# Performance work log

Hardware: AMD Instinct MI355X
Metric: run time of the kernel (lower is better)

The kernel has to match this reference:

```python
import jax, jax.numpy as jnp
import numpy as np

N, E = 50000, 400000          # nodes, edges
T, R = 4, 8                   # node types, relations (edge types)
H, DK = 8, 32                 # heads, head dim
DIN = DOUT = 256              # in/out feature dim (DOUT = H*DK)
SQRT_DK = float(np.sqrt(DK))


def setup_inputs() -> dict:
    key = jax.random.key(0)
    ks = jax.random.split(key, 12)
    f32 = jnp.float32
    return {
        "x": jax.random.normal(ks[0], (N, DIN), f32),
        "node_type": jax.random.randint(ks[1], (N,), 0, T, jnp.int32),
        "src": jax.random.randint(ks[2], (E,), 0, N, jnp.int32),
        "dst": jax.random.randint(ks[3], (E,), 0, N, jnp.int32),
        "etype": jax.random.randint(ks[4], (E,), 0, R, jnp.int32),
        "Wk": jax.random.normal(ks[5], (T, DOUT, DIN), f32) / np.sqrt(DIN).astype(np.float32),
        "bk": jnp.zeros((T, DOUT), f32),
        "Wq": jax.random.normal(ks[6], (T, DOUT, DIN), f32) / np.sqrt(DIN).astype(np.float32),
        "bq": jnp.zeros((T, DOUT), f32),
        "Wv": jax.random.normal(ks[7], (T, DOUT, DIN), f32) / np.sqrt(DIN).astype(np.float32),
        "bv": jnp.zeros((T, DOUT), f32),
        "Wa": jax.random.normal(ks[8], (T, DOUT, DOUT), f32) / np.sqrt(DOUT).astype(np.float32),
        "ba": jnp.zeros((T, DOUT), f32),
        "rel_pri": jnp.ones((R, H), f32),
        "rel_att": jax.random.normal(ks[9], (R, H, DK, DK), f32) / np.sqrt(DK).astype(np.float32),  # ~xavier
        "rel_msg": jax.random.normal(ks[10], (R, H, DK, DK), f32) / np.sqrt(DK).astype(np.float32),
        "skip": jnp.ones((T,), f32),
    }


def _typed_linear(h, W, b, ntype):
    # per-node-type linear: y_n = W[type_n] @ h_n + b[type_n]
    y = jnp.einsum('ni,tdi->ntd', h, W)                      # [N,T,D] (T is small)
    y = jnp.take_along_axis(y, ntype[:, None, None], axis=1)[:, 0]
    return y + b[ntype]


def _hgt_forward(x, node_type, src, dst, etype,
                 Wk, bk, Wq, bq, Wv, bv, Wa, ba,
                 rel_pri, rel_att, rel_msg, skip):
    # typed k/q/v projections -> [N,H,DK]
    K = _typed_linear(x, Wk, bk, node_type).reshape(N, H, DK)
    Q = _typed_linear(x, Wq, bq, node_type).reshape(N, H, DK)
    V = _typed_linear(x, Wv, bv, node_type).reshape(N, H, DK)

    k_e, q_e, v_e = K[src], Q[dst], V[src]                   # [E,H,DK] gathers

    # per-relation head transforms (loop over small fixed R, masked accumulate)
    key_e = jnp.zeros_like(k_e)
    msg_e = jnp.zeros_like(v_e)
    for r in range(R):
        m = (etype == r)[:, None, None].astype(x.dtype)
        key_e = key_e + m * jnp.einsum('ehd,hdf->ehf', k_e, rel_att[r])
        msg_e = msg_e + m * jnp.einsum('ehd,hdf->ehf', v_e, rel_msg[r])

    att = (q_e * key_e).sum(-1) * rel_pri[etype] / SQRT_DK   # [E,H]

    # softmax per (dst node, edge type) segment, then mean across edge types
    seg = dst * R + etype                                    # [E]
    S = N * R
    amax = jax.ops.segment_max(att, seg, num_segments=S)     # [S,H]
    ex = jnp.exp(att - amax[seg])
    denom = jax.ops.segment_sum(ex, seg, num_segments=S)
    w = ex / denom[seg]                                      # normalized attention [E,H]
    h_seg = jax.ops.segment_sum(w[:, :, None] * msg_e, seg, num_segments=S)  # [S,H,DK]
    cnt = jax.ops.segment_sum(jnp.ones((E,), x.dtype), seg, num_segments=S)  # [S]

    h_nr = h_seg.reshape(N, R, DOUT)
    present = (cnt.reshape(N, R) > 0).astype(x.dtype)        # which etypes hit each node
    t = h_nr.sum(1) / jnp.maximum(present.sum(1), 1.0)[:, None]  # cross_reducer='mean'

    trans = _typed_linear(t, Wa, ba, node_type)              # per-type output linear
    alpha = jax.nn.sigmoid(skip)[node_type][:, None]
    return trans * alpha + x * (1.0 - alpha)


def reference(x, node_type, src, dst, etype,
              Wk, bk, Wq, bq, Wv, bv, Wa, ba,
              rel_pri, rel_att, rel_msg, skip):
    return _hgt_forward(x, node_type, src, dst, etype,
                        Wk, bk, Wq, bq, Wv, bv, Wa, ba,
                        rel_pri, rel_att, rel_msg, skip)
```

## Files before the change

### kernel.cpp

```cpp
#include <hip/hip_runtime.h>
#include <math.h>
#include <stdint.h>

#define N_NODES 50000
#define N_EDGES 400000
#define N_T 4
#define N_R 8
#define N_H 8
#define DKD 32
#define D 256
#define TM 64
#define N_SEG (N_NODES * N_R)
#define EMASK 0xFFFFF
#define PROJ_BLOCKS ((N_NODES + TM - 1) / TM + N_T)

typedef _Float16 h2 __attribute__((ext_vector_type(2)));
typedef _Float16 v8h __attribute__((ext_vector_type(8)));
typedef float v4f __attribute__((ext_vector_type(4)));
typedef unsigned short u16;

__device__ __forceinline__ u16 h2u(_Float16 h) { return __builtin_bit_cast(u16, h); }
__device__ __forceinline__ h2 u2h2(unsigned int u) { return __builtin_bit_cast(h2, u); }

#if __has_builtin(__builtin_amdgcn_fdot2)
__device__ __forceinline__ float fdot2f(h2 a, h2 b, float c) {
    return __builtin_amdgcn_fdot2(a, b, c, false);
}
#else
__device__ __forceinline__ float fdot2f(h2 a, h2 b, float c) {
    return c + (float)a[0] * (float)b[0] + (float)a[1] * (float)b[1];
}
#endif

__device__ __forceinline__ float dot32h(const uint4* __restrict__ a,
                                        const uint4* __restrict__ q) {
    float s = 0.f;
    #pragma unroll
    for (int j = 0; j < 4; j++) {
        uint4 av = a[j], qv = q[j];
        s = fdot2f(u2h2(av.x), u2h2(qv.x), s);
        s = fdot2f(u2h2(av.y), u2h2(qv.y), s);
        s = fdot2f(u2h2(av.z), u2h2(qv.z), s);
        s = fdot2f(u2h2(av.w), u2h2(qv.w), s);
    }
    return s;
}

__global__ __launch_bounds__(256) void k_cvtW(
    const float4* __restrict__ w0, const float4* __restrict__ w1,
    const float4* __restrict__ w2, const float4* __restrict__ w3,
    ushort4* __restrict__ d, int n4each) {
    int i = blockIdx.x * 256 + threadIdx.x;
    if (i >= 4 * n4each) return;
    int sel = i / n4each, j = i - sel * n4each;
    const float4* s = (sel == 0) ? w0 : (sel == 1) ? w1 : (sel == 2) ? w2 : w3;
    float4 v = s[j];
    ushort4 o;
    o.x = h2u((_Float16)v.x); o.y = h2u((_Float16)v.y);
    o.z = h2u((_Float16)v.z); o.w = h2u((_Float16)v.w);
    d[i] = o;
}

__global__ __launch_bounds__(256) void k_cvt_att(const float4* __restrict__ s,
                                                 const float* __restrict__ pri,
                                                 ushort4* __restrict__ d, int n4) {
    int i = blockIdx.x * 256 + threadIdx.x;
    if (i >= n4) return;
    int mat = i >> 8;
    float sc = pri[mat] * 0.17677669529663687f;
    float4 v = s[i];
    ushort4 o;
    o.x = h2u((_Float16)(v.x * sc)); o.y = h2u((_Float16)(v.y * sc));
    o.z = h2u((_Float16)(v.z * sc)); o.w = h2u((_Float16)(v.w * sc));
    d[i] = o;
}

__global__ __launch_bounds__(256) void k_cvt_t(const float* __restrict__ s,
                                               u16* __restrict__ d) {
    int i = blockIdx.x * 256 + threadIdx.x;
    if (i >= N_R * N_H * DKD * DKD) return;
    int mat = i >> 10, w = i & 1023;
    int d0 = w >> 5, f = w & 31;
    d[(mat << 10) + f * DKD + d0] = h2u((_Float16)s[i]);
}

__global__ void k_hist(const int* __restrict__ nt, int* __restrict__ cnt) {
    int n = blockIdx.x * blockDim.x + threadIdx.x;
    if (n < N_NODES) atomicAdd(&cnt[nt[n]], 1);
}

__global__ void k_scan(const int* __restrict__ cnt, int* __restrict__ off,
                       int* __restrict__ toff) {
    int o = 0, to = 0;
    for (int t = 0; t < N_T; t++) {
        off[t] = o; toff[t] = to;
        o += cnt[t]; to += (cnt[t] + TM - 1) / TM;
    }
    off[N_T] = o; toff[N_T] = to;
}

__global__ void k_scatter(const int* __restrict__ nt, const int* __restrict__ off,
                          int* __restrict__ cur, int* __restrict__ order) {
    int n = blockIdx.x * blockDim.x + threadIdx.x;
    if (n >= N_NODES) return;
    int t = nt[n];
    int pos = off[t] + atomicAdd(&cur[t], 1);
    order[pos] = n;
}

__global__ void k_hist_seg(const int* __restrict__ dst, const int* __restrict__ et,
                           int* __restrict__ cnt) {
    int e = blockIdx.x * blockDim.x + threadIdx.x;
    if (e < N_EDGES) atomicAdd(&cnt[dst[e] * N_R + et[e]], 1);
}

__global__ __launch_bounds__(1024) void k_scan_l1(const int* __restrict__ cnt,
                                                  int* __restrict__ excl,
                                                  int* __restrict__ bsum) {
    __shared__ int sh[1024];
    int tid = threadIdx.x, i = blockIdx.x * 1024 + tid;
    int v = (i < N_SEG) ? cnt[i] : 0;
    sh[tid] = v;
    __syncthreads();
    #pragma unroll
    for (int ofs = 1; ofs < 1024; ofs <<= 1) {
        int t = (tid >= ofs) ? sh[tid - ofs] : 0;
        __syncthreads();
        sh[tid] += t;
        __syncthreads();
    }
    if (i < N_SEG) excl[i] = sh[tid] - v;
    if (tid == 1023) bsum[blockIdx.x] = sh[1023];
}

__global__ __launch_bounds__(512) void k_scan_l2(int* __restrict__ bsum, int NB) {
    __shared__ int sh[512];
    int tid = threadIdx.x;
    int v = (tid < NB) ? bsum[tid] : 0;
    sh[tid] = v;
    __syncthreads();
    #pragma unroll
    for (int ofs = 1; ofs < 512; ofs <<= 1) {
        int t = (tid >= ofs) ? sh[tid - ofs] : 0;
        __syncthreads();
        sh[tid] += t;
        __syncthreads();
    }
    if (tid < NB) bsum[tid] = sh[tid] - v;
}

__global__ void k_scan_l3(int* __restrict__ excl, const int* __restrict__ bsum) {
    int i = blockIdx.x * blockDim.x + threadIdx.x;
    if (i < N_SEG) excl[i] += bsum[i >> 10];
    else if (i == N_SEG) excl[N_SEG] = N_EDGES;
}

__global__ void k_scatter_seg(const int* __restrict__ src, const int* __restrict__ dst,
                              const int* __restrict__ et, const int* __restrict__ rp,
                              int* __restrict__ cur, int* __restrict__ esrc) {
    int e = blockIdx.x * blockDim.x + threadIdx.x;
    if (e >= N_EDGES) return;
    int r = et[e];
    int sg = dst[e] * N_R + r;
    int pos = rp[sg] + atomicAdd(&cur[sg], 1);
    esrc[pos] = src[e] | (r << 20);
}

__global__ __launch_bounds__(256) void k_proj(
    const float* __restrict__ x, const int* __restrict__ order,
    const int* __restrict__ off, const int* __restrict__ toff,
    const u16* __restrict__ Wkb, const float* __restrict__ bk,
    const u16* __restrict__ Wqb, const float* __restrict__ bq,
    const u16* __restrict__ Wvb, const float* __restrict__ bv,
    u16* __restrict__ Kb, u16* __restrict__ Qb, u16* __restrict__ Vb) {
    __shared__ __align__(16) u16 xs[TM][D + 8];
    int b = blockIdx.x;
    int t = -1;
    #pragma unroll
    for (int i = 0; i < N_T; i++)
        if (b >= toff[i] && b < toff[i + 1]) t = i;
    if (t < 0) return;
    int nodeBase = off[t] + (b - toff[t]) * TM;
    int count = min(TM, off[t + 1] - nodeBase);
    int tid = threadIdx.x;

    for (int j = tid; j < TM * (D / 4); j += 256) {
        int row = j >> 6, ch = j & 63;
        float4 v = {0.f, 0.f, 0.f, 0.f};
        if (row < count) {
            int g = order[nodeBase + row];
            v = *(const float4*)(x + (size_t)g * D + ch * 4);
        }
        ushort4 o;
        o.x = h2u((_Float16)v.x); o.y = h2u((_Float16)v.y);
        o.z = h2u((_Float16)v.z); o.w = h2u((_Float16)v.w);
        *(ushort4*)&xs[row][ch * 4] = o;
    }
    __syncthreads();

    int lane = tid & 63, wave = tid >> 6;
    int m = lane & 15, quad = lane >> 4;
    v8h a[8];
    #pragma unroll
    for (int ks = 0; ks < 8; ks++)
        a[ks] = *(const v8h*)&xs[wave * 16 + m][ks * 32 + quad * 8];

    int grow[4]; bool vrow[4];
    #pragma unroll
    for (int r = 0; r < 4; r++) {
        int rowi = wave * 16 + quad * 4 + r;
        vrow[r] = (rowi < count);
        grow[r] = vrow[r] ? order[nodeBase + rowi] : 0;
    }

    const u16* Ws[3] = {Wkb + (size_t)t * D * D, Wqb + (size_t)t * D * D, Wvb + (size_t)t * D * D};
    const float* Bs[3] = {bk + t * D, bq + t * D, bv + t * D};
    u16* Os[3] = {Kb, Qb, Vb};

    for (int p = 0; p < 3; p++) {
        const u16* W = Ws[p];
        for (int dt = 0; dt < 16; dt++) {
            int dcol = dt * 16 + m;
            v4f acc = {0.f, 0.f, 0.f, 0.f};
            #pragma unroll
            for (int ks = 0; ks < 8; ks++) {
                v8h bf = *(const v8h*)(W + (size_t)dcol * D + ks * 32 + quad * 8);
                acc = __builtin_amdgcn_mfma_f32_16x16x32_f16(a[ks], bf, acc, 0, 0, 0);
            }
            float bias = Bs[p][dcol];
            #pragma unroll
            for (int r = 0; r < 4; r++) {
                if (vrow[r])
                    Os[p][(size_t)grow[r] * D + dcol] = h2u((_Float16)(acc[r] + bias));
            }
        }
    }
}

__global__ __launch_bounds__(256, 4) void k_fused(
    const u16* __restrict__ Kb, u16* QTb, const u16* __restrict__ Vb,
    const int* __restrict__ rowptr, const int* __restrict__ esrc,
    const u16* __restrict__ Ab, const u16* __restrict__ Mtb) {
    __shared__ __align__(16) unsigned int Uldu[4][N_H][20];
    int wave = threadIdx.x >> 6, lane = threadIdx.x & 63;
    int n = blockIdx.x * 4 + wave;
    if (n >= N_NODES) return;
    int h = lane >> 3, fl = lane & 7, fo = fl * 4;
    int base = n * N_R;

    int bnd[N_R + 1];
    #pragma unroll
    for (int i = 0; i <= N_R; i++) bnd[i] = rowptr[base + i];

    uint4 qv4[4];
    {
        const uint4* qp = (const uint4*)(QTb + (size_t)n * D + h * DKD);
        #pragma unroll
        for (int j = 0; j < 4; j++) qv4[j] = qp[j];
    }

    h2 qt2[N_R][2];
    int np = 0;
    #pragma unroll
    for (int r = 0; r < N_R; r++) {
        if (bnd[r] >= bnd[r + 1]) continue;
        np++;
        const u16* Ar = Ab + ((size_t)(r * N_H + h) * DKD + fo) * DKD;
        float q0 = dot32h((const uint4*)(Ar), qv4);
        float q1 = dot32h((const uint4*)(Ar + DKD), qv4);
        float q2 = dot32h((const uint4*)(Ar + 2 * DKD), qv4);
        float q3 = dot32h((const uint4*)(Ar + 3 * DKD), qv4);
        qt2[r][0] = h2{(_Float16)q0, (_Float16)q1};
        qt2[r][1] = h2{(_Float16)q2, (_Float16)q3};
    }

    float den[N_R] = {0.f, 0.f, 0.f, 0.f, 0.f, 0.f, 0.f, 0.f};
    float ua[N_R][4] = {};

#define DOTQ(P, RS, KU) { \
    h2 _ka = u2h2((KU).x), _kb = u2h2((KU).y); \
    switch (RS) { \
    case 0: P = fdot2f(_kb, qt2[0][1], fdot2f(_ka, qt2[0][0], 0.f)); break; \
    case 1: P = fdot2f(_kb, qt2[1][1], fdot2f(_ka, qt2[1][0], 0.f)); break; \
    case 2: P = fdot2f(_kb, qt2[2][1], fdot2f(_ka, qt2[2][0], 0.f)); break; \
    case 3: P = fdot2f(_kb, qt2[3][1], fdot2f(_ka, qt2[3][0], 0.f)); break; \
    case 4: P = fdot2f(_kb, qt2[4][1], fdot2f(_ka, qt2[4][0], 0.f)); break; \
    case 5: P = fdot2f(_kb, qt2[5][1], fdot2f(_ka, qt2[5][0], 0.f)); break; \
    case 6: P = fdot2f(_kb, qt2[6][1], fdot2f(_ka, qt2[6][0], 0.f)); break; \
    default: P = fdot2f(_kb, qt2[7][1], fdot2f(_ka, qt2[7][0], 0.f)); break; } }

#define ACCR(R, EX, V0, V1, V2, V3) \
    den[R] += EX; ua[R][0] += EX*V0; ua[R][1] += EX*V1; ua[R][2] += EX*V2; ua[R][3] += EX*V3;

#define ACCE(RS, EX, VU) { \
    h2 _va = u2h2((VU).x), _vb = u2h2((VU).y); \
    float _v0 = (float)_va[0], _v1 = (float)_va[1]; \
    float _v2 = (float)_vb[0], _v3 = (float)_vb[1]; \
    switch (RS) { \
    case 0: ACCR(0, EX, _v0, _v1, _v2, _v3) break; \
    case 1: ACCR(1, EX, _v0, _v1, _v2, _v3) break; \
    case 2: ACCR(2, EX, _v0, _v1, _v2, _v3) break; \
    case 3: ACCR(3, EX, _v0, _v1, _v2, _v3) break; \
    case 4: ACCR(4, EX, _v0, _v1, _v2, _v3) break; \
    case 5: ACCR(5, EX, _v0, _v1, _v2, _v3) break; \
    case 6: ACCR(6, EX, _v0, _v1, _v2, _v3) break; \
    default: ACCR(7, EX, _v0, _v1, _v2, _v3) break; } }

    int eb = bnd[0], ee = bnd[N_R];
    size_t hoff = (size_t)(h * DKD + fo);
    for (int w0 = eb; w0 < ee; w0 += 64) {
        int wcnt = min(64, ee - w0);
        int myek = (lane < wcnt) ? esrc[w0 + lane] : 0;
        for (int i0 = 0; i0 < wcnt; i0 += 4) {
            int mc = wcnt - i0;
            int pk0 = __shfl(myek, i0);
            int pk1 = __shfl(myek, i0 + (mc > 1 ? 1 : 0));
            int pk2 = __shfl(myek, i0 + (mc > 2 ? 2 : 0));
            int pk3 = __shfl(myek, i0 + (mc > 3 ? 3 : 0));
            int s0 = pk0 & EMASK, s1 = pk1 & EMASK, s2 = pk2 & EMASK, s3 = pk3 & EMASK;
            int r0 = __builtin_amdgcn_readfirstlane(pk0) >> 20;
            int r1 = __builtin_amdgcn_readfirstlane(pk1) >> 20;
            int r2 = __builtin_amdgcn_readfirstlane(pk2) >> 20;
            int r3 = __builtin_amdgcn_readfirstlane(pk3) >> 20;
            uint2 ku0 = *(const uint2*)(Kb + (size_t)s0 * D + hoff);
            uint2 ku1 = *(const uint2*)(Kb + (size_t)s1 * D + hoff);
            uint2 ku2 = *(const uint2*)(Kb + (size_t)s2 * D + hoff);
            uint2 ku3 = *(const uint2*)(Kb + (size_t)s3 * D + hoff);
            uint2 vu0 = *(const uint2*)(Vb + (size_t)s0 * D + hoff);
            uint2 vu1 = *(const uint2*)(Vb + (size_t)s1 * D + hoff);
            uint2 vu2 = *(const uint2*)(Vb + (size_t)s2 * D + hoff);
            uint2 vu3 = *(const uint2*)(Vb + (size_t)s3 * D + hoff);
            float p0, p1, p2, p3;
            DOTQ(p0, r0, ku0);
            DOTQ(p1, r1, ku1);
            DOTQ(p2, r2, ku2);
            DOTQ(p3, r3, ku3);
            p0 += __shfl_xor(p0, 1); p1 += __shfl_xor(p1, 1);
            p2 += __shfl_xor(p2, 1); p3 += __shfl_xor(p3, 1);
            p0 += __shfl_xor(p0, 2); p1 += __shfl_xor(p1, 2);
            p2 += __shfl_xor(p2, 2); p3 += __shfl_xor(p3, 2);
            p0 += __shfl_xor(p0, 4); p1 += __shfl_xor(p1, 4);
            p2 += __shfl_xor(p2, 4); p3 += __shfl_xor(p3, 4);
            float ex0 = __expf(p0), ex1 = __expf(p1);
            float ex2 = __expf(p2), ex3 = __expf(p3);
            ACCE(r0, ex0, vu0);
            if (mc > 1) { ACCE(r1, ex1, vu1); }
            if (mc > 2) { ACCE(r2, ex2, vu2); }
            if (mc > 3) { ACCE(r3, ex3, vu3); }
        }
    }

    float macc[4] = {0.f, 0.f, 0.f, 0.f};
    #pragma unroll
    for (int r = 0; r < N_R; r++) {
        if (bnd[r] >= bnd[r + 1]) continue;
        float invd = 1.f / den[r];
        unsigned int pw0 = __builtin_bit_cast(unsigned int,
            h2{(_Float16)(ua[r][0] * invd), (_Float16)(ua[r][1] * invd)});
        unsigned int pw1 = __builtin_bit_cast(unsigned int,
            h2{(_Float16)(ua[r][2] * invd), (_Float16)(ua[r][3] * invd)});
        __builtin_amdgcn_wave_barrier();
        *(uint2*)&Uldu[wave][h][fl * 2] = uint2{pw0, pw1};
        __builtin_amdgcn_wave_barrier();
        uint4 Um[4];
        #pragma unroll
        for (int j = 0; j < 4; j++)
            Um[j] = *(const uint4*)&Uldu[wave][h][4 * j];
        const u16* mp = Mtb + ((size_t)(r * N_H + h) * DKD + fo) * DKD;
        #pragma unroll
        for (int j = 0; j < 4; j++)
            macc[j] += dot32h((const uint4*)(mp + j * DKD), Um);
        __builtin_amdgcn_wave_barrier();
    }

    float invp = (np > 0) ? 1.f / (float)np : 1.f;
    ushort4 o;
    o.x = h2u((_Float16)(macc[0] * invp)); o.y = h2u((_Float16)(macc[1] * invp));
    o.z = h2u((_Float16)(macc[2] * invp)); o.w = h2u((_Float16)(macc[3] * invp));
    *(ushort4*)(QTb + (size_t)n * D + hoff) = o;
}

__global__ __launch_bounds__(256) void k_out(
    const u16* __restrict__ TBF, const float* __restrict__ x,
    const int* __restrict__ order, const int* __restrict__ off, const int* __restrict__ toff,
    const u16* __restrict__ Wab, const float* __restrict__ ba,
    const float* __restrict__ skip, float* __restrict__ out) {
    __shared__ __align__(16) u16 xs[TM][D + 8];
    int b = blockIdx.x;
    int t = -1;
    #pragma unroll
    for (int i = 0; i < N_T; i++)
        if (b >= toff[i] && b < toff[i + 1]) t = i;
    if (t < 0) return;
    int nodeBase = off[t] + (b - toff[t]) * TM;
    int count = min(TM, off[t + 1] - nodeBase);
    int tid = threadIdx.x;

    for (int j = tid; j < TM * 32; j += 256) {
        int row = j >> 5, ch = j & 31;
        ushort4 z = {0, 0, 0, 0};
        if (row < count) {
            int g = order[nodeBase + row];
            const ushort4* p = (const ushort4*)(TBF + (size_t)g * D + ch * 8);
            *(ushort4*)&xs[row][ch * 8] = p[0];
            *(ushort4*)&xs[row][ch * 8 + 4] = p[1];
        } else {
            *(ushort4*)&xs[row][ch * 8] = z;
            *(ushort4*)&xs[row][ch * 8 + 4] = z;
        }
    }
    __syncthreads();

    int lane = tid & 63, wave = tid >> 6;
    int m = lane & 15, quad = lane >> 4;
    v8h a[8];
    #pragma unroll
    for (int ks = 0; ks < 8; ks++)
        a[ks] = *(const v8h*)&xs[wave * 16 + m][ks * 32 + quad * 8];

    int grow[4]; bool vrow[4];
    #pragma unroll
    for (int r = 0; r < 4; r++) {
        int rowi = wave * 16 + quad * 4 + r;
        vrow[r] = (rowi < count);
        grow[r] = vrow[r] ? order[nodeBase + rowi] : 0;
    }

    float sv = skip[t];
    float alpha = 1.f / (1.f + __expf(-sv));
    float beta = 1.f - alpha;
    const u16* W = Wab + (size_t)t * D * D;

    for (int dt = 0; dt < 16; dt++) {
        int dcol = dt * 16 + m;
        v4f acc = {0.f, 0.f, 0.f, 0.f};
        #pragma unroll
        for (int ks = 0; ks < 8; ks++) {
            v8h bf = *(const v8h*)(W + (size_t)dcol * D + ks * 32 + quad * 8);
            acc = __builtin_amdgcn_mfma_f32_16x16x32_f16(a[ks], bf, acc, 0, 0, 0);
        }
        float bias = ba[t * D + dcol];
        #pragma unroll
        for (int r = 0; r < 4; r++) {
            if (vrow[r]) {
                size_t o = (size_t)grow[r] * D + dcol;
                out[o] = alpha * (acc[r] + bias) + beta * x[o];
            }
        }
    }
}

extern "C" void kernel_launch(void* const* d_in, const int* in_sizes, int n_in,
                              void* d_out, int out_size, void* d_ws, size_t ws_size,
                              hipStream_t stream) {
    const float* x       = (const float*)d_in[0];
    const int* node_type = (const int*)d_in[1];
    const int* src       = (const int*)d_in[2];
    const int* dst       = (const int*)d_in[3];
    const int* etype     = (const int*)d_in[4];
    const float* Wk = (const float*)d_in[5];
    const float* bk = (const float*)d_in[6];
    const float* Wq = (const float*)d_in[7];
    const float* bq = (const float*)d_in[8];
    const float* Wv = (const float*)d_in[9];
    const float* bv = (const float*)d_in[10];
    const float* Wa = (const float*)d_in[11];
    const float* ba = (const float*)d_in[12];
    const float* rel_pri = (const float*)d_in[13];
    const float* rel_att = (const float*)d_in[14];
    const float* rel_msg = (const float*)d_in[15];
    const float* skip    = (const float*)d_in[16];
    float* out = (float*)d_out;
    char* ws = (char*)d_ws;

    const size_t SZH = (size_t)N_NODES * D * 2;
    const size_t WSZ = (size_t)N_T * D * D;
    const size_t RSZ = (size_t)N_R * N_H * DKD * DKD;
    u16* Kb  = (u16*)(ws);
    u16* Qb  = (u16*)(ws + SZH);
    u16* Vb  = (u16*)(ws + 2 * SZH);
    u16* TBF = Qb;
    u16* Wkb = (u16*)(ws + 3 * SZH);
    u16* Wqb = Wkb + WSZ;
    u16* Wvb = Wqb + WSZ;
    u16* Wab = Wvb + WSZ;
    u16* Ab  = Wab + WSZ;
    u16* Mtb = Ab + RSZ;
    int* order = (int*)(Mtb + RSZ);
    int* small = order + N_NODES;
    int* cnt  = small;
    int* cur  = small + 4;
    int* offp = small + 8;
    int* toffp= small + 13;

    char* ob = (char*)d_out;
    int* rowptr_seg = (int*)ob;
    int* cnt_seg    = rowptr_seg + (N_SEG + 16);
    int* cur_seg    = cnt_seg + N_SEG;
    int* esrc       = cur_seg + N_SEG;
    int* bsum       = esrc + N_EDGES;

    hipMemsetAsync(small, 0, 8 * sizeof(int), stream);
    hipMemsetAsync(cnt_seg, 0, 2 * (size_t)N_SEG * sizeof(int), stream);

    k_cvtW<<<(4 * (WSZ / 4) + 255) / 256, 256, 0, stream>>>(
        (const float4*)Wk, (const float4*)Wq, (const float4*)Wv, (const float4*)Wa,
        (ushort4*)Wkb, WSZ / 4);
    k_cvt_att<<<(RSZ / 4 + 255) / 256, 256, 0, stream>>>(
        (const float4*)rel_att, rel_pri, (ushort4*)Ab, RSZ / 4);
    k_cvt_t<<<(RSZ + 255) / 256, 256, 0, stream>>>(rel_msg, Mtb);

    k_hist<<<(N_NODES + 255) / 256, 256, 0, stream>>>(node_type, cnt);
    k_scan<<<1, 1, 0, stream>>>(cnt, offp, toffp);
    k_scatter<<<(N_NODES + 255) / 256, 256, 0, stream>>>(node_type, offp, cur, order);

    const int NB = (N_SEG + 1023) / 1024;
    k_hist_seg<<<(N_EDGES + 255) / 256, 256, 0, stream>>>(dst, etype, cnt_seg);
    k_scan_l1<<<NB, 1024, 0, stream>>>(cnt_seg, rowptr_seg, bsum);
    k_scan_l2<<<1, 512, 0, stream>>>(bsum, NB);
    k_scan_l3<<<(N_SEG + 1 + 255) / 256, 256, 0, stream>>>(rowptr_seg, bsum);
    k_scatter_seg<<<(N_EDGES + 255) / 256, 256, 0, stream>>>(src, dst, etype,
                                                             rowptr_seg, cur_seg, esrc);

    k_proj<<<PROJ_BLOCKS, 256, 0, stream>>>(x, order, offp, toffp,
                                            Wkb, bk, Wqb, bq, Wvb, bv, Kb, Qb, Vb);

    k_fused<<<(N_NODES + 3) / 4, 256, 0, stream>>>(Kb, Qb, Vb, rowptr_seg, esrc,
                                                   Ab, Mtb);

    k_out<<<PROJ_BLOCKS, 256, 0, stream>>>(TBF, x, order, offp, toffp,
                                           Wab, ba, skip, out);
}
```

Measured before the change: 2.042 ms.

## Remap fused attention kernel to one thread per node-head with full-vector work

Rewrites the fused edge-attention kernel so each thread owns a whole (node, head) pair and processes its 32-dim q-transform, K·q dots, softmax accumulation and message transform serially per relation segment. Previously eight lanes split each head's dimensions and relied on shuffles, LDS staging and relation-indexed switch tables. The relation id is no longer packed into esrc, and exp2 is used with a log2(e) factor folded into the attention scale. The new mapping removes cross-lane reductions but raises per-thread register use (32-element U and macc arrays plus the Q4 vectors) and lowers thread count, which risks occupancy loss and uncoalesced 64-byte per-thread gathers.

Measured after the change: 2.248 ms. 1.1x slower.

```diff
diff --git a/kernel.cpp b/kernel.cpp
--- a/kernel.cpp
+++ b/kernel.cpp
@@ -11,7 +11,6 @@
 #define D 256
 #define TM 64
 #define N_SEG (N_NODES * N_R)
-#define EMASK 0xFFFFF
 #define PROJ_BLOCKS ((N_NODES + TM - 1) / TM + N_T)
 
 typedef _Float16 h2 __attribute__((ext_vector_type(2)));
@@ -32,17 +31,35 @@
 }
 #endif
 
-__device__ __forceinline__ float dot32h(const uint4* __restrict__ a,
-                                        const uint4* __restrict__ q) {
+__device__ __forceinline__ unsigned int pk16(float a, float b) {
+#if __has_builtin(__builtin_amdgcn_cvt_pkrtz)
+    return __builtin_bit_cast(unsigned int, __builtin_amdgcn_cvt_pkrtz(a, b));
+#else
+    return __builtin_bit_cast(unsigned int, h2{(_Float16)a, (_Float16)b});
+#endif
+}
+
+struct Q4 { uint4 a, b, c, d; };
+
+__device__ __forceinline__ float dot32q(const uint4* __restrict__ m, const Q4& q) {
+    uint4 m0 = m[0], m1 = m[1], m2 = m[2], m3 = m[3];
     float s = 0.f;
-    #pragma unroll
-    for (int j = 0; j < 4; j++) {
-        uint4 av = a[j], qv = q[j];
-        s = fdot2f(u2h2(av.x), u2h2(qv.x), s);
-        s = fdot2f(u2h2(av.y), u2h2(qv.y), s);
-        s = fdot2f(u2h2(av.z), u2h2(qv.z), s);
-        s = fdot2f(u2h2(av.w), u2h2(qv.w), s);
-    }
+    s = fdot2f(u2h2(m0.x), u2h2(q.a.x), s);
+    s = fdot2f(u2h2(m0.y), u2h2(q.a.y), s);
+    s = fdot2f(u2h2(m0.z), u2h2(q.a.z), s);
+    s = fdot2f(u2h2(m0.w), u2h2(q.a.w), s);
+    s = fdot2f(u2h2(m1.x), u2h2(q.b.x), s);
+    s = fdot2f(u2h2(m1.y), u2h2(q.b.y), s);
+    s = fdot2f(u2h2(m1.z), u2h2(q.b.z), s);
+    s = fdot2f(u2h2(m1.w), u2h2(q.b.w), s);
+    s = fdot2f(u2h2(m2.x), u2h2(q.c.x), s);
+    s = fdot2f(u2h2(m2.y), u2h2(q.c.y), s);
+    s = fdot2f(u2h2(m2.z), u2h2(q.c.z), s);
+    s = fdot2f(u2h2(m2.w), u2h2(q.c.w), s);
+    s = fdot2f(u2h2(m3.x), u2h2(q.d.x), s);
+    s = fdot2f(u2h2(m3.y), u2h2(q.d.y), s);
+    s = fdot2f(u2h2(m3.z), u2h2(q.d.z), s);
+    s = fdot2f(u2h2(m3.w), u2h2(q.d.w), s);
     return s;
 }
 
@@ -67,7 +84,7 @@
     int i = blockIdx.x * 256 + threadIdx.x;
     if (i >= n4) return;
     int mat = i >> 8;
-    float sc = pri[mat] * 0.17677669529663687f;
+    float sc = pri[mat] * 0.2550309305920868f;
     float4 v = s[i];
     ushort4 o;
     o.x = h2u((_Float16)(v.x * sc)); o.y = h2u((_Float16)(v.y * sc));
@@ -160,10 +177,9 @@
                               int* __restrict__ cur, int* __restrict__ esrc) {
     int e = blockIdx.x * blockDim.x + threadIdx.x;
     if (e >= N_EDGES) return;
-    int r = et[e];
-    int sg = dst[e] * N_R + r;
+    int sg = dst[e] * N_R + et[e];
     int pos = rp[sg] + atomicAdd(&cur[sg], 1);
-    esrc[pos] = src[e] | (r << 20);
+    esrc[pos] = src[e];
 }
 
 __global__ __launch_bounds__(256) void k_proj(
@@ -237,147 +253,135 @@
     }
 }
 
-__global__ __launch_bounds__(256, 4) void k_fused(
+__global__ __launch_bounds__(256) void k_fused(
     const u16* __restrict__ Kb, u16* QTb, const u16* __restrict__ Vb,
     const int* __restrict__ rowptr, const int* __restrict__ esrc,
     const u16* __restrict__ Ab, const u16* __restrict__ Mtb) {
-    __shared__ __align__(16) unsigned int Uldu[4][N_H][20];
-    int wave = threadIdx.x >> 6, lane = threadIdx.x & 63;
-    int n = blockIdx.x * 4 + wave;
+    int tid = threadIdx.x;
+    int n = blockIdx.x * 32 + (tid >> 3);
     if (n >= N_NODES) return;
-    int h = lane >> 3, fl = lane & 7, fo = fl * 4;
+    int h = tid & 7;
     int base = n * N_R;
-
-    int bnd[N_R + 1];
-    #pragma unroll
-    for (int i = 0; i <= N_R; i++) bnd[i] = rowptr[base + i];
-
-    uint4 qv4[4];
-    {
-        const uint4* qp = (const uint4*)(QTb + (size_t)n * D + h * DKD);
-        #pragma unroll
-        for (int j = 0; j < 4; j++) qv4[j] = qp[j];
-    }
-
-    h2 qt2[N_R][2];
-    int np = 0;
-    #pragma unroll
+    u16* qrow = QTb + (size_t)n * D + h * DKD;
+
+    float macc[DKD];
+    #pragma unroll
+    for (int j = 0; j < DKD; j++) macc[j] = 0.f;
+    float np = 0.f;
+
+    int s0 = rowptr[base];
     for (int r = 0; r < N_R; r++) {
-        if (bnd[r] >= bnd[r + 1]) continue;
-        np++;
-        const u16* Ar = Ab + ((size_t)(r * N_H + h) * DKD + fo) * DKD;
-        float q0 = dot32h((const uint4*)(Ar), qv4);
-        float q1 = dot32h((const uint4*)(Ar + DKD), qv4);
-        float q2 = dot32h((const uint4*)(Ar + 2 * DKD), qv4);
-        float q3 = dot32h((const uint4*)(Ar + 3 * DKD), qv4);
-        qt2[r][0] = h2{(_Float16)q0, (_Float16)q1};
-        qt2[r][1] = h2{(_Float16)q2, (_Float16)q3};
-    }
-
-    float den[N_R] = {0.f, 0.f, 0.f, 0.f, 0.f, 0.f, 0.f, 0.f};
-    float ua[N_R][4] = {};
-
-#define DOTQ(P, RS, KU) { \
-    h2 _ka = u2h2((KU).x), _kb = u2h2((KU).y); \
-    switch (RS) { \
-    case 0: P = fdot2f(_kb, qt2[0][1], fdot2f(_ka, qt2[0][0], 0.f)); break; \
-    case 1: P = fdot2f(_kb, qt2[1][1], fdot2f(_ka, qt2[1][0], 0.f)); break; \
-    case 2: P = fdot2f(_kb, qt2[2][1], fdot2f(_ka, qt2[2][0], 0.f)); break; \
-    case 3: P = fdot2f(_kb, qt2[3][1], fdot2f(_ka, qt2[3][0], 0.f)); break; \
-    case 4: P = fdot2f(_kb, qt2[4][1], fdot2f(_ka, qt2[4][0], 0.f)); break; \
-    case 5: P = fdot2f(_kb, qt2[5][1], fdot2f(_ka, qt2[5][0], 0.f)); break; \
-    case 6: P = fdot2f(_kb, qt2[6][1], fdot2f(_ka, qt2[6][0], 0.f)); break; \
-    default: P = fdot2f(_kb, qt2[7][1], fdot2f(_ka, qt2[7][0], 0.f)); break; } }
-
-#define ACCR(R, EX, V0, V1, V2, V3) \
-    den[R] += EX; ua[R][0] += EX*V0; ua[R][1] += EX*V1; ua[R][2] += EX*V2; ua[R][3] += EX*V3;
-
-#define ACCE(RS, EX, VU) { \
-    h2 _va = u2h2((VU).x), _vb = u2h2((VU).y); \
-    float _v0 = (float)_va[0], _v1 = (float)_va[1]; \
-    float _v2 = (float)_vb[0], _v3 = (float)_vb[1]; \
-    switch (RS) { \
-    case 0: ACCR(0, EX, _v0, _v1, _v2, _v3) break; \
-    case 1: ACCR(1, EX, _v0, _v1, _v2, _v3) break; \
-    case 2: ACCR(2, EX, _v0, _v1, _v2, _v3) break; \
-    case 3: ACCR(3, EX, _v0, _v1, _v2, _v3) break; \
-    case 4: ACCR(4, EX, _v0, _v1, _v2, _v3) break; \
-    case 5: ACCR(5, EX, _v0, _v1, _v2, _v3) break; \
-    case 6: ACCR(6, EX, _v0, _v1, _v2, _v3) break; \
-    default: ACCR(7, EX, _v0, _v1, _v2, _v3) break; } }
-
-    int eb = bnd[0], ee = bnd[N_R];
-    size_t hoff = (size_t)(h * DKD + fo);
-    for (int w0 = eb; w0 < ee; w0 += 64) {
-        int wcnt = min(64, ee - w0);
-        int myek = (lane < wcnt) ? esrc[w0 + lane] : 0;
-        for (int i0 = 0; i0 < wcnt; i0 += 4) {
-            int mc = wcnt - i0;
-            int pk0 = __shfl(myek, i0);
-            int pk1 = __shfl(myek, i0 + (mc > 1 ? 1 : 0));
-            int pk2 = __shfl(myek, i0 + (mc > 2 ? 2 : 0));
-            int pk3 = __shfl(myek, i0 + (mc > 3 ? 3 : 0));
-            int s0 = pk0 & EMASK, s1 = pk1 & EMASK, s2 = pk2 & EMASK, s3 = pk3 & EMASK;
-            int r0 = __builtin_amdgcn_readfirstlane(pk0) >> 20;
-            int r1 = __builtin_amdgcn_readfirstlane(pk1) >> 20;
-            int r2 = __builtin_amdgcn_readfirstlane(pk2) >> 20;
-            int r3 = __builtin_amdgcn_readfirstlane(pk3) >> 20;
-            uint2 ku0 = *(const uint2*)(Kb + (size_t)s0 * D + hoff);
-            uint2 ku1 = *(const uint2*)(Kb + (size_t)s1 * D + hoff);
-            uint2 ku2 = *(const uint2*)(Kb + (size_t)s2 * D + hoff);
-            uint2 ku3 = *(const uint2*)(Kb + (size_t)s3 * D + hoff);
-            uint2 vu0 = *(const uint2*)(Vb + (size_t)s0 * D + hoff);
-            uint2 vu1 = *(const uint2*)(Vb + (size_t)s1 * D + hoff);
-            uint2 vu2 = *(const uint2*)(Vb + (size_t)s2 * D + hoff);
-            uint2 vu3 = *(const uint2*)(Vb + (size_t)s3 * D + hoff);
-            float p0, p1, p2, p3;
-            DOTQ(p0, r0, ku0);
-            DOTQ(p1, r1, ku1);
-            DOTQ(p2, r2, ku2);
-            DOTQ(p3, r3, ku3);
-            p0 += __shfl_xor(p0, 1); p1 += __shfl_xor(p1, 1);
-            p2 += __shfl_xor(p2, 1); p3 += __shfl_xor(p3, 1);
-            p0 += __shfl_xor(p0, 2); p1 += __shfl_xor(p1, 2);
-            p2 += __shfl_xor(p2, 2); p3 += __shfl_xor(p3, 2);
-            p0 += __shfl_xor(p0, 4); p1 += __shfl_xor(p1, 4);
-            p2 += __shfl_xor(p2, 4); p3 += __shfl_xor(p3, 4);
-            float ex0 = __expf(p0), ex1 = __expf(p1);
-            float ex2 = __expf(p2), ex3 = __expf(p3);
-            ACCE(r0, ex0, vu0);
-            if (mc > 1) { ACCE(r1, ex1, vu1); }
-            if (mc > 2) { ACCE(r2, ex2, vu2); }
-            if (mc > 3) { ACCE(r3, ex3, vu3); }
+        int s1 = rowptr[base + r + 1];
+        if (s0 < s1) {
+            np += 1.f;
+            Q4 q4;
+            {
+                const uint4* qp = (const uint4*)qrow;
+                q4.a = qp[0]; q4.b = qp[1]; q4.c = qp[2]; q4.d = qp[3];
+            }
+            const uint4* Ar = (const uint4*)(Ab + ((size_t)(r * N_H + h) << 10));
+            Q4 qt;
+            {
+                float t0, t1;
+                t0 = dot32q(Ar + 0, q4);  t1 = dot32q(Ar + 4, q4);  qt.a.x = pk16(t0, t1);
+                t0 = dot32q(Ar + 8, q4);  t1 = dot32q(Ar + 12, q4); qt.a.y = pk16(t0, t1);
+                t0 = dot32q(Ar + 16, q4); t1 = dot32q(Ar + 20, q4); qt.a.z = pk16(t0, t1);
+                t0 = dot32q(Ar + 24, q4); t1 = dot32q(Ar + 28, q4); qt.a.w = pk16(t0, t1);
+                t0 = dot32q(Ar + 32, q4); t1 = dot32q(Ar + 36, q4); qt.b.x = pk16(t0, t1);
+                t0 = dot32q(Ar + 40, q4); t1 = dot32q(Ar + 44, q4); qt.b.y = pk16(t0, t1);
+                t0 = dot32q(Ar + 48, q4); t1 = dot32q(Ar + 52, q4); qt.b.z = pk16(t0, t1);
+                t0 = dot32q(Ar + 56, q4); t1 = dot32q(Ar + 60, q4); qt.b.w = pk16(t0, t1);
+                t0 = dot32q(Ar + 64, q4); t1 = dot32q(Ar + 68, q4); qt.c.x = pk16(t0, t1);
+                t0 = dot32q(Ar + 72, q4); t1 = dot32q(Ar + 76, q4); qt.c.y = pk16(t0, t1);
+                t0 = dot32q(Ar + 80, q4); t1 = dot32q(Ar + 84, q4); qt.c.z = pk16(t0, t1);
+                t0 = dot32q(Ar + 88, q4); t1 = dot32q(Ar + 92, q4); qt.c.w = pk16(t0, t1);
+                t0 = dot32q(Ar + 96, q4); t1 = dot32q(Ar + 100, q4); qt.d.x = pk16(t0, t1);
+                t0 = dot32q(Ar + 104, q4); t1 = dot32q(Ar + 108, q4); qt.d.y = pk16(t0, t1);
+                t0 = dot32q(Ar + 112, q4); t1 = dot32q(Ar + 116, q4); qt.d.z = pk16(t0, t1);
+                t0 = dot32q(Ar + 120, q4); t1 = dot32q(Ar + 124, q4); qt.d.w = pk16(t0, t1);
+            }
+            float den = 0.f;
+            float U[DKD];
+            #pragma unroll
+            for (int j = 0; j < DKD; j++) U[j] = 0.f;
+            for (int e = s0; e < s1; e++) {
+                int s = esrc[e];
+                const uint4* kp = (const uint4*)(Kb + (size_t)s * D + h * DKD);
+                const uint4* vp = (const uint4*)(Vb + (size_t)s * D + h * DKD);
+                Q4 kv; kv.a = kp[0]; kv.b = kp[1]; kv.c = kp[2]; kv.d = kp[3];
+                uint4 v0 = vp[0], v1 = vp[1], v2 = vp[2], v3 = vp[3];
+                float p = 0.f;
+                p = fdot2f(u2h2(kv.a.x), u2h2(qt.a.x), p);
+                p = fdot2f(u2h2(kv.a.y), u2h2(qt.a.y), p);
+                p = fdot2f(u2h2(kv.a.z), u2h2(qt.a.z), p);
+                p = fdot2f(u2h2(kv.a.w), u2h2(qt.a.w), p);
+                p = fdot2f(u2h2(kv.b.x), u2h2(qt.b.x), p);
+                p = fdot2f(u2h2(kv.b.y), u2h2(qt.b.y), p);
+                p = fdot2f(u2h2(kv.b.z), u2h2(qt.b.z), p);
+                p = fdot2f(u2h2(kv.b.w), u2h2(qt.b.w), p);
+                p = fdot2f(u2h2(kv.c.x), u2h2(qt.c.x), p);
+                p = fdot2f(u2h2(kv.c.y), u2h2(qt.c.y), p);
+                p = fdot2f(u2h2(kv.c.z), u2h2(qt.c.z), p);
+                p = fdot2f(u2h2(kv.c.w), u2h2(qt.c.w), p);
+                p = fdot2f(u2h2(kv.d.x), u2h2(qt.d.x), p);
+                p = fdot2f(u2h2(kv.d.y), u2h2(qt.d.y), p);
+                p = fdot2f(u2h2(kv.d.z), u2h2(qt.d.z), p);
+                p = fdot2f(u2h2(kv.d.w), u2h2(qt.d.w), p);
+                float ex = exp2f(p);
+                den += ex;
+#define UACC(VV, J0) { h2 _t = u2h2(VV); U[J0] += ex * (float)_t[0]; U[J0 + 1] += ex * (float)_t[1]; }
+                UACC(v0.x, 0)  UACC(v0.y, 2)  UACC(v0.z, 4)  UACC(v0.w, 6)
+                UACC(v1.x, 8)  UACC(v1.y, 10) UACC(v1.z, 12) UACC(v1.w, 14)
+                UACC(v2.x, 16) UACC(v2.y, 18) UACC(v2.z, 20) UACC(v2.w, 22)
+                UACC(v3.x, 24) UACC(v3.y, 26) UACC(v3.z, 28) UACC(v3.w, 30)
+#undef UACC
+            }
+            float invd = 1.f / den;
+            Q4 uh;
+            uh.a.x = pk16(U[0] * invd, U[1] * invd);
+            uh.a.y = pk16(U[2] * invd, U[3] * invd);
+            uh.a.z = pk16(U[4] * invd, U[5] * invd);
+            uh.a.w = pk16(U[6] * invd, U[7] * invd);
+            uh.b.x = pk16(U[8] * invd, U[9] * invd);
+            uh.b.y = pk16(U[10] * invd, U[11] * invd);
+            uh.b.z = pk16(U[12] * invd, U[13] * invd);
+            uh.b.w = pk16(U[14] * invd, U[15] * invd);
+            uh.c.x = pk16(U[16] * invd, U[17] * invd);
+            uh.c.y = pk16(U[18] * invd, U[19] * invd);
+            uh.c.z = pk16(U[20] * invd, U[21] * invd);
+            uh.c.w = pk16(U[22] * invd, U[23] * invd);
+            uh.d.x = pk16(U[24] * invd, U[25] * invd);
+            uh.d.y = pk16(U[26] * invd, U[27] * invd);
+            uh.d.z = pk16(U[28] * invd, U[29] * invd);
+            uh.d.w = pk16(U[30] * invd, U[31] * invd);
+            const uint4* Mr = (const uint4*)(Mtb + ((size_t)(r * N_H + h) << 10));
+            #pragma unroll
+            for (int f = 0; f < DKD; f++)
+                macc[f] += dot32q(Mr + f * 4, uh);
         }
-    }
-
-    float macc[4] = {0.f, 0.f, 0.f, 0.f};
-    #pragma unroll
-    for (int r = 0; r < N_R; r++) {
-        if (bnd[r] >= bnd[r + 1]) continue;
-        float invd = 1.f / den[r];
-        unsigned int pw0 = __builtin_bit_cast(unsigned int,
-            h2{(_Float16)(ua[r][0] * invd), (_Float16)(ua[r][1] * invd)});
-        unsigned int pw1 = __builtin_bit_cast(unsigned int,
-            h2{(_Float16)(ua[r][2] * invd), (_Float16)(ua[r][3] * invd)});
-        __builtin_amdgcn_wave_barrier();
-        *(uint2*)&Uldu[wave][h][fl * 2] = uint2{pw0, pw1};
-        __builtin_amdgcn_wave_barrier();
-        uint4 Um[4];
-        #pragma unroll
-        for (int j = 0; j < 4; j++)
-            Um[j] = *(const uint4*)&Uldu[wave][h][4 * j];
-        const u16* mp = Mtb + ((size_t)(r * N_H + h) * DKD + fo) * DKD;
-        #pragma unroll
-        for (int j = 0; j < 4; j++)
-            macc[j] += dot32h((const uint4*)(mp + j * DKD), Um);
-        __builtin_amdgcn_wave_barrier();
-    }
-
-    float invp = (np > 0) ? 1.f / (float)np : 1.f;
-    ushort4 o;
-    o.x = h2u((_Float16)(macc[0] * invp)); o.y = h2u((_Float16)(macc[1] * invp));
-    o.z = h2u((_Float16)(macc[2] * invp)); o.w = h2u((_Float16)(macc[3] * invp));
-    *(ushort4*)(QTb + (size_t)n * D + hoff) = o;
+        s0 = s1;
+    }
+
+    float invp = (np > 0.f) ? 1.f / np : 1.f;
+    uint4 o0, o1, o2, o3;
+    o0.x = pk16(macc[0] * invp, macc[1] * invp);
+    o0.y = pk16(macc[2] * invp, macc[3] * invp);
+    o0.z = pk16(macc[4] * invp, macc[5] * invp);
+    o0.w = pk16(macc[6] * invp, macc[7] * invp);
+    o1.x = pk16(macc[8] * invp, macc[9] * invp);
+    o1.y = pk16(macc[10] * invp, macc[11] * invp);
+    o1.z = pk16(macc[12] * invp, macc[13] * invp);
+    o1.w = pk16(macc[14] * invp, macc[15] * invp);
+    o2.x = pk16(macc[16] * invp, macc[17] * invp);
+    o2.y = pk16(macc[18] * invp, macc[19] * invp);
+    o2.z = pk16(macc[20] * invp, macc[21] * invp);
+    o2.w = pk16(macc[22] * invp, macc[23] * invp);
+    o3.x = pk16(macc[24] * invp, macc[25] * invp);
+    o3.y = pk16(macc[26] * invp, macc[27] * invp);
+    o3.z = pk16(macc[28] * invp, macc[29] * invp);
+    o3.w = pk16(macc[30] * invp, macc[31] * invp);
+    uint4* op = (uint4*)qrow;
+    op[0] = o0; op[1] = o1; op[2] = o2; op[3] = o3;
 }
 
 __global__ __launch_bounds__(256) void k_out(
@@ -525,8 +529,8 @@
     k_proj<<<PROJ_BLOCKS, 256, 0, stream>>>(x, order, offp, toffp,
                                             Wkb, bk, Wqb, bq, Wvb, bv, Kb, Qb, Vb);
 
-    k_fused<<<(N_NODES + 3) / 4, 256, 0, stream>>>(Kb, Qb, Vb, rowptr_seg, esrc,
-                                                   Ab, Mtb);
+    k_fused<<<(N_NODES + 31) / 32, 256, 0, stream>>>(Kb, Qb, Vb, rowptr_seg, esrc,
+                                                     Ab, Mtb);
 
     k_out<<<PROJ_BLOCKS, 256, 0, stream>>>(TBF, x, order, offp, toffp,
                                            Wab, ba, skip, out);
```

## Replace per-relation segment CSR with per-node CSR, presence bitmask and compact edge arrays

Applied to the files above, without the earlier changes.

Edges are now grouped by destination node only, not by (node, relation). A per-node bitmask of which relations are present is packed into the high byte of the node's row offset. This shrinks the histogram, scan and memset work from N*R entries to N entries. Edge sources are stored as 16-bit indices and relations as 8-bit values, in a buffer carved out of the no-longer-needed K/Q/V weight region after projection, which cuts index traffic in the fused kernel. Other changes: log2(e) is folded into the attention scale so exp2f replaces expf, fp16 packing uses cvt_pkrtz, and the occupancy hint on the fused kernel is dropped. The risks are register pressure once the hint is gone and the fact that 16-bit indices only hold while the node count fits in 16 bits.

Result: no change. 2.010 ms (-1.6%).

```diff
diff --git a/kernel.cpp b/kernel.cpp
--- a/kernel.cpp
+++ b/kernel.cpp
@@ -10,14 +10,13 @@
 #define DKD 32
 #define D 256
 #define TM 64
-#define N_SEG (N_NODES * N_R)
-#define EMASK 0xFFFFF
 #define PROJ_BLOCKS ((N_NODES + TM - 1) / TM + N_T)
 
 typedef _Float16 h2 __attribute__((ext_vector_type(2)));
 typedef _Float16 v8h __attribute__((ext_vector_type(8)));
 typedef float v4f __attribute__((ext_vector_type(4)));
 typedef unsigned short u16;
+typedef unsigned char u8;
 
 __device__ __forceinline__ u16 h2u(_Float16 h) { return __builtin_bit_cast(u16, h); }
 __device__ __forceinline__ h2 u2h2(unsigned int u) { return __builtin_bit_cast(h2, u); }
@@ -31,6 +30,14 @@
     return c + (float)a[0] * (float)b[0] + (float)a[1] * (float)b[1];
 }
 #endif
+
+__device__ __forceinline__ unsigned int pk16(float a, float b) {
+#if __has_builtin(__builtin_amdgcn_cvt_pkrtz)
+    return __builtin_bit_cast(unsigned int, __builtin_amdgcn_cvt_pkrtz(a, b));
+#else
+    return __builtin_bit_cast(unsigned int, h2{(_Float16)a, (_Float16)b});
+#endif
+}
 
 __device__ __forceinline__ float dot32h(const uint4* __restrict__ a,
                                         const uint4* __restrict__ q) {
@@ -67,7 +74,7 @@
     int i = blockIdx.x * 256 + threadIdx.x;
     if (i >= n4) return;
     int mat = i >> 8;
-    float sc = pri[mat] * 0.17677669529663687f;
+    float sc = pri[mat] * 0.2550309305920868f;
     float4 v = s[i];
     ushort4 o;
     o.x = h2u((_Float16)(v.x * sc)); o.y = h2u((_Float16)(v.y * sc));
@@ -108,18 +115,21 @@
     order[pos] = n;
 }
 
-__global__ void k_hist_seg(const int* __restrict__ dst, const int* __restrict__ et,
-                           int* __restrict__ cnt) {
+__global__ void k_hist2(const int* __restrict__ dst, const int* __restrict__ et,
+                        int* __restrict__ cnt2, int* __restrict__ presw) {
     int e = blockIdx.x * blockDim.x + threadIdx.x;
-    if (e < N_EDGES) atomicAdd(&cnt[dst[e] * N_R + et[e]], 1);
-}
-
-__global__ __launch_bounds__(1024) void k_scan_l1(const int* __restrict__ cnt,
-                                                  int* __restrict__ excl,
+    if (e >= N_EDGES) return;
+    int d = dst[e];
+    atomicAdd(&cnt2[d], 1);
+    atomicOr(&presw[d], 1 << et[e]);
+}
+
+__global__ __launch_bounds__(1024) void k_scan_l1(const int* __restrict__ cnt2,
+                                                  int* __restrict__ nbase,
                                                   int* __restrict__ bsum) {
     __shared__ int sh[1024];
     int tid = threadIdx.x, i = blockIdx.x * 1024 + tid;
-    int v = (i < N_SEG) ? cnt[i] : 0;
+    int v = (i < N_NODES) ? cnt2[i] : 0;
     sh[tid] = v;
     __syncthreads();
     #pragma unroll
@@ -129,7 +139,7 @@
         sh[tid] += t;
         __syncthreads();
     }
-    if (i < N_SEG) excl[i] = sh[tid] - v;
+    if (i < N_NODES) nbase[i] = sh[tid] - v;
     if (tid == 1023) bsum[blockIdx.x] = sh[1023];
 }
 
@@ -149,21 +159,25 @@
     if (tid < NB) bsum[tid] = sh[tid] - v;
 }
 
-__global__ void k_scan_l3(int* __restrict__ excl, const int* __restrict__ bsum) {
+__global__ void k_scan_l3(int* __restrict__ nbase, const int* __restrict__ bsum,
+                          const int* __restrict__ presw) {
     int i = blockIdx.x * blockDim.x + threadIdx.x;
-    if (i < N_SEG) excl[i] += bsum[i >> 10];
-    else if (i == N_SEG) excl[N_SEG] = N_EDGES;
-}
-
-__global__ void k_scatter_seg(const int* __restrict__ src, const int* __restrict__ dst,
-                              const int* __restrict__ et, const int* __restrict__ rp,
-                              int* __restrict__ cur, int* __restrict__ esrc) {
+    if (i < N_NODES)
+        nbase[i] = (nbase[i] + bsum[i >> 10]) | (presw[i] << 24);
+    else if (i == N_NODES)
+        nbase[N_NODES] = N_EDGES;
+}
+
+__global__ void k_scatter2(const int* __restrict__ src, const int* __restrict__ dst,
+                           const int* __restrict__ et, const int* __restrict__ nbase,
+                           int* __restrict__ cur2,
+                           u16* __restrict__ esrc16, u8* __restrict__ er8) {
     int e = blockIdx.x * blockDim.x + threadIdx.x;
     if (e >= N_EDGES) return;
-    int r = et[e];
-    int sg = dst[e] * N_R + r;
-    int pos = rp[sg] + atomicAdd(&cur[sg], 1);
-    esrc[pos] = src[e] | (r << 20);
+    int d = dst[e];
+    int pos = (nbase[d] & 0xFFFFFF) + atomicAdd(&cur2[d], 1);
+    esrc16[pos] = (u16)src[e];
+    er8[pos] = (u8)et[e];
 }
 
 __global__ __launch_bounds__(256) void k_proj(
@@ -237,20 +251,21 @@
     }
 }
 
-__global__ __launch_bounds__(256, 4) void k_fused(
+__global__ __launch_bounds__(256) void k_fused(
     const u16* __restrict__ Kb, u16* QTb, const u16* __restrict__ Vb,
-    const int* __restrict__ rowptr, const int* __restrict__ esrc,
+    const int* __restrict__ nbase, const u16* __restrict__ esrc16,
+    const u8* __restrict__ er8,
     const u16* __restrict__ Ab, const u16* __restrict__ Mtb) {
     __shared__ __align__(16) unsigned int Uldu[4][N_H][20];
     int wave = threadIdx.x >> 6, lane = threadIdx.x & 63;
     int n = blockIdx.x * 4 + wave;
     if (n >= N_NODES) return;
     int h = lane >> 3, fl = lane & 7, fo = fl * 4;
-    int base = n * N_R;
-
-    int bnd[N_R + 1];
-    #pragma unroll
-    for (int i = 0; i <= N_R; i++) bnd[i] = rowptr[base + i];
+
+    int w0v = nbase[n], w1v = nbase[n + 1];
+    int s0 = __builtin_amdgcn_readfirstlane(w0v) & 0xFFFFFF;
+    int s1 = __builtin_amdgcn_readfirstlane(w1v) & 0xFFFFFF;
+    int pres = (__builtin_amdgcn_readfirstlane(w0v) >> 24) & 0xFF;
 
     uint4 qv4[4];
     {
@@ -260,11 +275,8 @@
     }
 
     h2 qt2[N_R][2];
-    int np = 0;
-    #pragma unroll
     for (int r = 0; r < N_R; r++) {
-        if (bnd[r] >= bnd[r + 1]) continue;
-        np++;
+        if (!(pres & (1 << r))) continue;
         const u16* Ar = Ab + ((size_t)(r * N_H + h) * DKD + fo) * DKD;
         float q0 = dot32h((const uint4*)(Ar), qv4);
         float q1 = dot32h((const uint4*)(Ar + DKD), qv4);
@@ -306,30 +318,32 @@
     case 6: ACCR(6, EX, _v0, _v1, _v2, _v3) break; \
     default: ACCR(7, EX, _v0, _v1, _v2, _v3) break; } }
 
-    int eb = bnd[0], ee = bnd[N_R];
     size_t hoff = (size_t)(h * DKD + fo);
-    for (int w0 = eb; w0 < ee; w0 += 64) {
-        int wcnt = min(64, ee - w0);
-        int myek = (lane < wcnt) ? esrc[w0 + lane] : 0;
+    for (int w0 = s0; w0 < s1; w0 += 64) {
+        int wcnt = min(64, s1 - w0);
+        int myek = 0;
+        if (lane < wcnt)
+            myek = (int)esrc16[w0 + lane] | ((int)er8[w0 + lane] << 20);
         for (int i0 = 0; i0 < wcnt; i0 += 4) {
             int mc = wcnt - i0;
             int pk0 = __shfl(myek, i0);
             int pk1 = __shfl(myek, i0 + (mc > 1 ? 1 : 0));
             int pk2 = __shfl(myek, i0 + (mc > 2 ? 2 : 0));
             int pk3 = __shfl(myek, i0 + (mc > 3 ? 3 : 0));
-            int s0 = pk0 & EMASK, s1 = pk1 & EMASK, s2 = pk2 & EMASK, s3 = pk3 & EMASK;
+            int s0e = pk0 & 0xFFFFF, s1e = pk1 & 0xFFFFF;
+            int s2e = pk2 & 0xFFFFF, s3e = pk3 & 0xFFFFF;
             int r0 = __builtin_amdgcn_readfirstlane(pk0) >> 20;
             int r1 = __builtin_amdgcn_readfirstlane(pk1) >> 20;
             int r2 = __builtin_amdgcn_readfirstlane(pk2) >> 20;
             int r3 = __builtin_amdgcn_readfirstlane(pk3) >> 20;
-            uint2 ku0 = *(const uint2*)(Kb + (size_t)s0 * D + hoff);
-            uint2 ku1 = *(const uint2*)(Kb + (size_t)s1 * D + hoff);
-            uint2 ku2 = *(const uint2*)(Kb + (size_t)s2 * D + hoff);
-            uint2 ku3 = *(const uint2*)(Kb + (size_t)s3 * D + hoff);
-            uint2 vu0 = *(const uint2*)(Vb + (size_t)s0 * D + hoff);
-            uint2 vu1 = *(const uint2*)(Vb + (size_t)s1 * D + hoff);
-            uint2 vu2 = *(const uint2*)(Vb + (size_t)s2 * D + hoff);
-            uint2 vu3 = *(const uint2*)(Vb + (size_t)s3 * D + hoff);
+            uint2 ku0 = *(const uint2*)(Kb + (size_t)s0e * D + hoff);
+            uint2 ku1 = *(const uint2*)(Kb + (size_t)s1e * D + hoff);
+            uint2 ku2 = *(const uint2*)(Kb + (size_t)s2e * D + hoff);
+            uint2 ku3 = *(const uint2*)(Kb + (size_t)s3e * D + hoff);
+            uint2 vu0 = *(const uint2*)(Vb + (size_t)s0e * D + hoff);
+            uint2 vu1 = *(const uint2*)(Vb + (size_t)s1e * D + hoff);
+            uint2 vu2 = *(const uint2*)(Vb + (size_t)s2e * D + hoff);
+            uint2 vu3 = *(const uint2*)(Vb + (size_t)s3e * D + hoff);
             float p0, p1, p2, p3;
             DOTQ(p0, r0, ku0);
             DOTQ(p1, r1, ku1);
@@ -341,8 +355,8 @@
             p2 += __shfl_xor(p2, 2); p3 += __shfl_xor(p3, 2);
             p0 += __shfl_xor(p0, 4); p1 += __shfl_xor(p1, 4);
             p2 += __shfl_xor(p2, 4); p3 += __shfl_xor(p3, 4);
-            float ex0 = __expf(p0), ex1 = __expf(p1);
-            float ex2 = __expf(p2), ex3 = __expf(p3);
+            float ex0 = exp2f(p0), ex1 = exp2f(p1);
+            float ex2 = exp2f(p2), ex3 = exp2f(p3);
             ACCE(r0, ex0, vu0);
             if (mc > 1) { ACCE(r1, ex1, vu1); }
             if (mc > 2) { ACCE(r2, ex2, vu2); }
@@ -353,12 +367,10 @@
     float macc[4] = {0.f, 0.f, 0.f, 0.f};
     #pragma unroll
     for (int r = 0; r < N_R; r++) {
-        if (bnd[r] >= bnd[r + 1]) continue;
+        if (!(pres & (1 << r))) continue;
         float invd = 1.f / den[r];
-        unsigned int pw0 = __builtin_bit_cast(unsigned int,
-            h2{(_Float16)(ua[r][0] * invd), (_Float16)(ua[r][1] * invd)});
-        unsigned int pw1 = __builtin_bit_cast(unsigned int,
-            h2{(_Float16)(ua[r][2] * invd), (_Float16)(ua[r][3] * invd)});
+        unsigned int pw0 = pk16(ua[r][0] * invd, ua[r][1] * invd);
+        unsigned int pw1 = pk16(ua[r][2] * invd, ua[r][3] * invd);
         __builtin_amdgcn_wave_barrier();
         *(uint2*)&Uldu[wave][h][fl * 2] = uint2{pw0, pw1};
         __builtin_amdgcn_wave_barrier();
@@ -373,6 +385,7 @@
         __builtin_amdgcn_wave_barrier();
     }
 
+    int np = __popc(pres);
     float invp = (np > 0) ? 1.f / (float)np : 1.f;
     ushort4 o;
     o.x = h2u((_Float16)(macc[0] * invp)); o.y = h2u((_Float16)(macc[1] * invp));
@@ -493,15 +506,18 @@
     int* offp = small + 8;
     int* toffp= small + 13;
 
+    u16* esrc16 = Wkb;
+    u8*  er8    = (u8*)(esrc16 + N_EDGES);
+    int* nbase  = (int*)(er8 + N_EDGES);
+
     char* ob = (char*)d_out;
-    int* rowptr_seg = (int*)ob;
-    int* cnt_seg    = rowptr_seg + (N_SEG + 16);
-    int* cur_seg    = cnt_seg + N_SEG;
-    int* esrc       = cur_seg + N_SEG;
-    int* bsum       = esrc + N_EDGES;
+    int* cnt2  = (int*)ob;
+    int* cur2  = cnt2 + N_NODES;
+    int* presw = cur2 + N_NODES;
+    int* bsum  = presw + N_NODES;
 
     hipMemsetAsync(small, 0, 8 * sizeof(int), stream);
-    hipMemsetAsync(cnt_seg, 0, 2 * (size_t)N_SEG * sizeof(int), stream);
+    hipMemsetAsync(cnt2, 0, 3 * (size_t)N_NODES * sizeof(int), stream);
 
     k_cvtW<<<(4 * (WSZ / 4) + 255) / 256, 256, 0, stream>>>(
         (const float4*)Wk, (const float4*)Wq, (const float4*)Wv, (const float4*)Wa,
@@ -514,18 +530,18 @@
     k_scan<<<1, 1, 0, stream>>>(cnt, offp, toffp);
     k_scatter<<<(N_NODES + 255) / 256, 256, 0, stream>>>(node_type, offp, cur, order);
 
-    const int NB = (N_SEG + 1023) / 1024;
-    k_hist_seg<<<(N_EDGES + 255) / 256, 256, 0, stream>>>(dst, etype, cnt_seg);
-    k_scan_l1<<<NB, 1024, 0, stream>>>(cnt_seg, rowptr_seg, bsum);
-    k_scan_l2<<<1, 512, 0, stream>>>(bsum, NB);
-    k_scan_l3<<<(N_SEG + 1 + 255) / 256, 256, 0, stream>>>(rowptr_seg, bsum);
-    k_scatter_seg<<<(N_EDGES + 255) / 256, 256, 0, stream>>>(src, dst, etype,
-                                                             rowptr_seg, cur_seg, esrc);
-
     k_proj<<<PROJ_BLOCKS, 256, 0, stream>>>(x, order, offp, toffp,
                                             Wkb, bk, Wqb, bq, Wvb, bv, Kb, Qb, Vb);
 
-    k_fused<<<(N_NODES + 3) / 4, 256, 0, stream>>>(Kb, Qb, Vb, rowptr_seg, esrc,
+    const int NB = (N_NODES + 1023) / 1024;
+    k_hist2<<<(N_EDGES + 255) / 256, 256, 0, stream>>>(dst, etype, cnt2, presw);
+    k_scan_l1<<<NB, 1024, 0, stream>>>(cnt2, nbase, bsum);
+    k_scan_l2<<<1, 512, 0, stream>>>(bsum, NB);
+    k_scan_l3<<<(N_NODES + 1 + 255) / 256, 256, 0, stream>>>(nbase, bsum, presw);
+    k_scatter2<<<(N_EDGES + 255) / 256, 256, 0, stream>>>(src, dst, etype, nbase,
+                                                          cur2, esrc16, er8);
+
+    k_fused<<<(N_NODES + 3) / 4, 256, 0, stream>>>(Kb, Qb, Vb, nbase, esrc16, er8,
                                                    Ab, Mtb);
 
     k_out<<<PROJ_BLOCKS, 256, 0, stream>>>(TBF, x, order, offp, toffp,
```
